# Performance work log

Measured on AMD Instinct MI355X. Metric: run time of the kernel, lower is better.

Reference implementation:

```python
import jax, jax.numpy as jnp
import numpy as np


def setup_inputs() -> dict:
    key = jax.random.key(0)
    k1, k2, k3 = jax.random.split(key, 3)
    B, C, Q, E = 32, 2048, 128, 200
    x_contexts = jax.random.normal(k1, (B, C, E), dtype=jnp.float32)
    x_questions = jax.random.normal(k2, (B, Q, E), dtype=jnp.float32)
    # weight of nn.Linear(3E, 1, bias=False), flattened to (3E,)
    w_sim = jax.random.normal(k3, (3 * E,), dtype=jnp.float32) * (1.0 / np.sqrt(3 * E))
    return {"x_contexts": x_contexts, "x_questions": x_questions, "w_sim": w_sim}


def reference(x_contexts, x_questions, w_sim):
    # x_contexts: [B,C,E], x_questions: [B,Q,E], w_sim: [3E]
    E = x_contexts.shape[-1]
    w1, w2, w3 = w_sim[:E], w_sim[E:2 * E], w_sim[2 * E:]
    # Trilinear similarity S[b,c,q] = w1.c + w2.q + w3.(c*q), decomposed so the
    # [B,C,Q,3E] tensor of the original expand+cat+linear is never materialized.
    s_c = jnp.einsum('bce,e->bc', x_contexts, w1)              # [B,C]
    s_q = jnp.einsum('bqe,e->bq', x_questions, w2)             # [B,Q]
    s_cq = jnp.einsum('bce,bqe->bcq', x_contexts * w3, x_questions)  # [B,C,Q]
    S = s_cq + s_c[:, :, None] + s_q[:, None, :]               # [B,C,Q]

    # Context-to-question: row softmax over Q, then attend over questions.
    c2q = jnp.einsum('bcq,bqe->bce', jax.nn.softmax(S, axis=-1), x_questions)

    # Question-to-context: max over Q, softmax over C, attend over contexts.
    q2c_w = jax.nn.softmax(jnp.max(S, axis=-1), axis=-1)       # [B,C]
    q2c = jnp.einsum('bc,bce->be', q2c_w, x_contexts)          # [B,E]
    q2c = q2c[:, None, :]                                      # broadcast to [B,C,E]

    return jnp.concatenate(
        [x_contexts, c2q, x_contexts * c2q, x_contexts * q2c], axis=-1)  # [B,C,4E]
```

## Files before the change

kernel.cpp:

```cpp
#include <hip/hip_runtime.h>

#define B_ 32
#define C_ 2048
#define Q_ 128
#define E_ 200
#define TB 32

typedef __attribute__((ext_vector_type(4))) float f32x4;

__global__ __launch_bounds__(256) void xqt_kernel(const float* __restrict__ xq,
                                                  float* __restrict__ xqT) {
    __shared__ float tl[32][33];
    const int blk = blockIdx.x;
    const int b  = blk / 28;
    const int r  = blk - b * 28;
    const int qt = r / 7, et = r - (r / 7) * 7;
    const int q0 = qt * 32, e0 = et * 32;
    const int tx = threadIdx.x & 31, ty = threadIdx.x >> 5;
    #pragma unroll
    for (int i = 0; i < 4; ++i) {
        const int q = q0 + ty + 8 * i, e = e0 + tx;
        if (e < E_) tl[ty + 8 * i][tx] = xq[((size_t)b * Q_ + q) * E_ + e];
    }
    __syncthreads();
    #pragma unroll
    for (int i = 0; i < 4; ++i) {
        const int e = e0 + ty + 8 * i, q = q0 + tx;
        if (e < E_) xqT[((size_t)b * E_ + e) * Q_ + q] = tl[tx][ty + 8 * i];
    }
}

__global__ __launch_bounds__(256) void sq_kernel(const float* __restrict__ xq,
                                                 const float* __restrict__ w,
                                                 float* __restrict__ sq) {
    const int wave = blockIdx.x * 4 + (threadIdx.x >> 6);
    const int lane = threadIdx.x & 63;
    const float* row = xq + (size_t)wave * E_;
    float a = 0.f;
    if (lane < 50) {
        const f32x4 v  = *(const f32x4*)&row[lane * 4];
        const f32x4 wv = *(const f32x4*)&w[E_ + lane * 4];
        a = (v.x * wv.x + v.y * wv.y) + (v.z * wv.z + v.w * wv.w);
    }
    #pragma unroll
    for (int off = 32; off; off >>= 1) a += __shfl_xor(a, off);
    if (lane == 0) sq[wave] = a;
}

__global__ __launch_bounds__(256) void row2_kernel(const float* __restrict__ xc_g,
                                                   const float* __restrict__ xq_g,
                                                   const float* __restrict__ xqT_g,
                                                   const float* __restrict__ w_g,
                                                   const float* __restrict__ sq_g,
                                                   float* __restrict__ m_g,
                                                   float* __restrict__ out) {
    __shared__ float scw3_l[TB][E_];
    __shared__ float P_l[TB][Q_];
    __shared__ float sc_l[TB];

    const int t    = threadIdx.x;
    const int b    = blockIdx.x >> 6;
    const int tile = blockIdx.x & 63;
    const int bc0  = b * C_ + tile * TB;

    {
        const int r  = t >> 3;
        const int k  = t & 7;
        const int e0 = k * 25;
        const float* xc_row = xc_g + (size_t)(bc0 + r) * E_;
        float p1 = 0.f;
        #pragma unroll
        for (int i = 0; i < 25; ++i) {
            const int e = e0 + i;
            const float v = xc_row[e];
            scw3_l[r][e] = v * w_g[2 * E_ + e];
            p1 = fmaf(v, w_g[e], p1);
        }
        p1 += __shfl_xor(p1, 1);
        p1 += __shfl_xor(p1, 2);
        p1 += __shfl_xor(p1, 4);
        if (k == 0) sc_l[r] = p1;
    }
    __syncthreads();

    const int qg = t & 31;
    const int cg = t >> 5;
    const int c4 = cg * 4;
    const int q4 = qg * 4;

    f32x4 acc[4] = {};
    const float* xqT_b = xqT_g + (size_t)b * E_ * Q_;
    for (int e = 0; e < E_; e += 4) {
        const f32x4 x0 = *(const f32x4*)&xqT_b[(e + 0) * Q_ + q4];
        const f32x4 x1 = *(const f32x4*)&xqT_b[(e + 1) * Q_ + q4];
        const f32x4 x2 = *(const f32x4*)&xqT_b[(e + 2) * Q_ + q4];
        const f32x4 x3 = *(const f32x4*)&xqT_b[(e + 3) * Q_ + q4];
        #pragma unroll
        for (int ci = 0; ci < 4; ++ci) {
            const f32x4 a = *(const f32x4*)&scw3_l[c4 + ci][e];
            acc[ci] += a.x * x0 + a.y * x1 + a.z * x2 + a.w * x3;
        }
    }

    const f32x4 sqv = *(const f32x4*)&sq_g[b * Q_ + q4];
    float mx[4], sm[4];
    #pragma unroll
    for (int ci = 0; ci < 4; ++ci) {
        acc[ci] += sc_l[c4 + ci] + sqv;
        mx[ci] = fmaxf(fmaxf(acc[ci].x, acc[ci].y), fmaxf(acc[ci].z, acc[ci].w));
    }
    #pragma unroll
    for (int off = 16; off; off >>= 1) {
        #pragma unroll
        for (int ci = 0; ci < 4; ++ci) mx[ci] = fmaxf(mx[ci], __shfl_xor(mx[ci], off));
    }
    if (qg == 0) {
        #pragma unroll
        for (int ci = 0; ci < 4; ++ci) m_g[bc0 + c4 + ci] = mx[ci];
    }
    #pragma unroll
    for (int ci = 0; ci < 4; ++ci) {
        f32x4 p;
        p.x = __expf(acc[ci].x - mx[ci]);
        p.y = __expf(acc[ci].y - mx[ci]);
        p.z = __expf(acc[ci].z - mx[ci]);
        p.w = __expf(acc[ci].w - mx[ci]);
        acc[ci] = p;
        sm[ci] = (p.x + p.y) + (p.z + p.w);
    }
    #pragma unroll
    for (int off = 16; off; off >>= 1) {
        #pragma unroll
        for (int ci = 0; ci < 4; ++ci) sm[ci] += __shfl_xor(sm[ci], off);
    }
    #pragma unroll
    for (int ci = 0; ci < 4; ++ci) {
        acc[ci] *= (1.f / sm[ci]);
        *(f32x4*)&P_l[c4 + ci][q4] = acc[ci];
    }
    __syncthreads();

    const float* xq_b = xq_g + (size_t)b * Q_ * E_;
    #pragma unroll
    for (int pass = 0; pass < 2; ++pass) {
        const int e4 = pass * 128 + q4;
        if (e4 < E_) {
            f32x4 o[4] = {};
            for (int q = 0; q < Q_; q += 4) {
                const f32x4 xv0 = *(const f32x4*)&xq_b[(q + 0) * E_ + e4];
                const f32x4 xv1 = *(const f32x4*)&xq_b[(q + 1) * E_ + e4];
                const f32x4 xv2 = *(const f32x4*)&xq_b[(q + 2) * E_ + e4];
                const f32x4 xv3 = *(const f32x4*)&xq_b[(q + 3) * E_ + e4];
                #pragma unroll
                for (int ci = 0; ci < 4; ++ci) {
                    const f32x4 p = *(const f32x4*)&P_l[c4 + ci][q];
                    o[ci] += p.x * xv0 + p.y * xv1 + p.z * xv2 + p.w * xv3;
                }
            }
            #pragma unroll
            for (int ci = 0; ci < 4; ++ci) {
                const size_t row = (size_t)(bc0 + c4 + ci);
                const f32x4 xcv = *(const f32x4*)&xc_g[row * E_ + e4];
                float* orow = out + row * (4 * E_);
                *(f32x4*)&orow[e4]          = xcv;
                *(f32x4*)&orow[E_ + e4]     = o[ci];
                *(f32x4*)&orow[2 * E_ + e4] = xcv * o[ci];
            }
        }
    }
}

__global__ __launch_bounds__(256) void q2c_partial(const float* __restrict__ xc_g,
                                                   const float* __restrict__ m_g,
                                                   float* __restrict__ part,
                                                   float* __restrict__ pmax,
                                                   float* __restrict__ psum) {
    __shared__ float wl[64];
    __shared__ float red;
    const int blk = blockIdx.x;
    const int b = blk >> 5, g = blk & 31;
    const int t = threadIdx.x;
    const int c0 = g * 64;

    const float v = (t < 64) ? m_g[b * C_ + c0 + t] : -3.4e38f;
    if (t < 64) {
        float mxl = v;
        #pragma unroll
        for (int off = 32; off; off >>= 1) mxl = fmaxf(mxl, __shfl_xor(mxl, off));
        const float e = __expf(v - mxl);
        wl[t] = e;
        float s = e;
        #pragma unroll
        for (int off = 32; off; off >>= 1) s += __shfl_xor(s, off);
        if (t == 0) { pmax[blk] = mxl; psum[blk] = s; red = mxl; }
    }
    __syncthreads();

    if (t < E_) {
        float acc = 0.f;
        const float* base = xc_g + ((size_t)(b * C_ + c0)) * E_ + t;
        #pragma unroll 8
        for (int c = 0; c < 64; ++c) acc = fmaf(wl[c], base[(size_t)c * E_], acc);
        part[(size_t)blk * E_ + t] = acc;
    }
}

__global__ __launch_bounds__(256) void q2c_reduce(const float* __restrict__ part,
                                                  const float* __restrict__ pmax,
                                                  const float* __restrict__ psum,
                                                  float* __restrict__ q2c) {
    __shared__ float sc[32];
    __shared__ float inv_total;
    const int b = blockIdx.x, t = threadIdx.x;
    if (t < 64) {
        const float pm = (t < 32) ? pmax[b * 32 + t] : -3.4e38f;
        float M = pm;
        #pragma unroll
        for (int off = 32; off; off >>= 1) M = fmaxf(M, __shfl_xor(M, off));
        const float s = (t < 32) ? __expf(pm - M) : 0.f;
        float tot = (t < 32) ? psum[b * 32 + t] * s : 0.f;
        #pragma unroll
        for (int off = 32; off; off >>= 1) tot += __shfl_xor(tot, off);
        if (t < 32) sc[t] = s;
        if (t == 0) inv_total = 1.f / tot;
    }
    __syncthreads();
    if (t < E_) {
        float a = 0.f;
        #pragma unroll
        for (int g = 0; g < 32; ++g)
            a = fmaf(part[(size_t)(b * 32 + g) * E_ + t], sc[g], a);
        q2c[b * E_ + t] = a * inv_total;
    }
}

__global__ __launch_bounds__(256) void out4_kernel(const float* __restrict__ xc_g,
                                                   const float* __restrict__ q2c,
                                                   float* __restrict__ out) {
    const unsigned int idx = blockIdx.x * 256u + threadIdx.x;
    const unsigned int n = idx * 4u;
    const unsigned int e = n % E_;
    const unsigned int row = n / E_;
    const unsigned int b = row / C_;
    const f32x4 xcv = *(const f32x4*)&xc_g[n];
    const f32x4 qv  = *(const f32x4*)&q2c[b * E_ + e];
    *(f32x4*)&out[(size_t)row * (4 * E_) + 3 * E_ + e] = xcv * qv;
}

extern "C" void kernel_launch(void* const* d_in, const int* in_sizes, int n_in,
                              void* d_out, int out_size, void* d_ws, size_t ws_size,
                              hipStream_t stream) {
    const float* xc = (const float*)d_in[0];
    const float* xq = (const float*)d_in[1];
    const float* w  = (const float*)d_in[2];
    for (int i = 0; i < n_in; ++i) {
        if      (in_sizes[i] == B_ * C_ * E_) xc = (const float*)d_in[i];
        else if (in_sizes[i] == B_ * Q_ * E_) xq = (const float*)d_in[i];
        else if (in_sizes[i] == 3 * E_)       w  = (const float*)d_in[i];
    }
    float* out = (float*)d_out;

    float* ws    = (float*)d_ws;
    float* sq    = ws;
    float* m     = sq + B_ * Q_;
    float* q2c   = m + B_ * C_;
    float* xqT   = q2c + B_ * E_;
    float* part  = xqT;
    float* pmax  = xqT + 262144;
    float* psum  = xqT + 262144 + 2048;

    xqt_kernel  <<<B_ * 28,            256, 0, stream>>>(xq, xqT);
    sq_kernel   <<<B_ * Q_ / 4,        256, 0, stream>>>(xq, w, sq);
    row2_kernel <<<B_ * (C_ / TB),     256, 0, stream>>>(xc, xq, xqT, w, sq, m, out);
    q2c_partial <<<B_ * 32,            256, 0, stream>>>(xc, m, part, pmax, psum);
    q2c_reduce  <<<B_,                 256, 0, stream>>>(part, pmax, psum, q2c);
    out4_kernel <<<(B_ * C_ * E_ / 4) / 256, 256, 0, stream>>>(xc, q2c, out);
}
```

Measured before the change: 407.6 us.

## Merge prep kernels, halve row tile, fold q2c reduce into output kernel

The transpose and s_q kernels become one launch, with the block index choosing the role. The main row kernel tile drops from 32 to 16 context rows per block, doubling the block count for occupancy at the cost of less reuse of xqT and xq per block. The q2c softmax now computes the global max inside each partial block, which removes the rescale pass, and the separate reduce kernel is folded into the final output kernel. This cuts launches and removes a tiny serial kernel, but each q2c_partial block now rereads all 2048 maxima for its batch and each out4 block rereads all 32 partials.

After: 515.6 us. 26.5% more time.

```diff
diff --git a/kernel.cpp b/kernel.cpp
--- a/kernel.cpp
+++ b/kernel.cpp
@@ -4,47 +4,47 @@
 #define C_ 2048
 #define Q_ 128
 #define E_ 200
-#define TB 32
+#define TB 16
 
 typedef __attribute__((ext_vector_type(4))) float f32x4;
 
-__global__ __launch_bounds__(256) void xqt_kernel(const float* __restrict__ xq,
-                                                  float* __restrict__ xqT) {
+__global__ __launch_bounds__(256) void prep_kernel(const float* __restrict__ xq,
+                                                   const float* __restrict__ w,
+                                                   float* __restrict__ xqT,
+                                                   float* __restrict__ sq) {
     __shared__ float tl[32][33];
-    const int blk = blockIdx.x;
-    const int b  = blk / 28;
-    const int r  = blk - b * 28;
-    const int qt = r / 7, et = r - (r / 7) * 7;
-    const int q0 = qt * 32, e0 = et * 32;
-    const int tx = threadIdx.x & 31, ty = threadIdx.x >> 5;
-    #pragma unroll
-    for (int i = 0; i < 4; ++i) {
-        const int q = q0 + ty + 8 * i, e = e0 + tx;
-        if (e < E_) tl[ty + 8 * i][tx] = xq[((size_t)b * Q_ + q) * E_ + e];
-    }
-    __syncthreads();
-    #pragma unroll
-    for (int i = 0; i < 4; ++i) {
-        const int e = e0 + ty + 8 * i, q = q0 + tx;
-        if (e < E_) xqT[((size_t)b * E_ + e) * Q_ + q] = tl[tx][ty + 8 * i];
-    }
-}
-
-__global__ __launch_bounds__(256) void sq_kernel(const float* __restrict__ xq,
-                                                 const float* __restrict__ w,
-                                                 float* __restrict__ sq) {
-    const int wave = blockIdx.x * 4 + (threadIdx.x >> 6);
-    const int lane = threadIdx.x & 63;
-    const float* row = xq + (size_t)wave * E_;
-    float a = 0.f;
-    if (lane < 50) {
-        const f32x4 v  = *(const f32x4*)&row[lane * 4];
-        const f32x4 wv = *(const f32x4*)&w[E_ + lane * 4];
-        a = (v.x * wv.x + v.y * wv.y) + (v.z * wv.z + v.w * wv.w);
-    }
-    #pragma unroll
-    for (int off = 32; off; off >>= 1) a += __shfl_xor(a, off);
-    if (lane == 0) sq[wave] = a;
+    if (blockIdx.x < 896) {
+        const int blk = blockIdx.x;
+        const int b  = blk / 28;
+        const int r  = blk - b * 28;
+        const int qt = r / 7, et = r - (r / 7) * 7;
+        const int q0 = qt * 32, e0 = et * 32;
+        const int tx = threadIdx.x & 31, ty = threadIdx.x >> 5;
+        #pragma unroll
+        for (int i = 0; i < 4; ++i) {
+            const int q = q0 + ty + 8 * i, e = e0 + tx;
+            if (e < E_) tl[ty + 8 * i][tx] = xq[((size_t)b * Q_ + q) * E_ + e];
+        }
+        __syncthreads();
+        #pragma unroll
+        for (int i = 0; i < 4; ++i) {
+            const int e = e0 + ty + 8 * i, q = q0 + tx;
+            if (e < E_) xqT[((size_t)b * E_ + e) * Q_ + q] = tl[tx][ty + 8 * i];
+        }
+    } else {
+        const int wave = (blockIdx.x - 896) * 4 + (threadIdx.x >> 6);
+        const int lane = threadIdx.x & 63;
+        const float* row = xq + (size_t)wave * E_;
+        float a = 0.f;
+        if (lane < 50) {
+            const f32x4 v  = *(const f32x4*)&row[lane * 4];
+            const f32x4 wv = *(const f32x4*)&w[E_ + lane * 4];
+            a = (v.x * wv.x + v.y * wv.y) + (v.z * wv.z + v.w * wv.w);
+        }
+        #pragma unroll
+        for (int off = 32; off; off >>= 1) a += __shfl_xor(a, off);
+        if (lane == 0) sq[wave] = a;
+    }
 }
 
 __global__ __launch_bounds__(256) void row2_kernel(const float* __restrict__ xc_g,
@@ -59,18 +59,18 @@
     __shared__ float sc_l[TB];
 
     const int t    = threadIdx.x;
-    const int b    = blockIdx.x >> 6;
-    const int tile = blockIdx.x & 63;
+    const int b    = blockIdx.x >> 7;
+    const int tile = blockIdx.x & 127;
     const int bc0  = b * C_ + tile * TB;
 
     {
-        const int r  = t >> 3;
-        const int k  = t & 7;
-        const int e0 = k * 25;
+        const int r   = t >> 4;
+        const int k   = t & 15;
+        const int e0  = (k < 8) ? k * 13 : 104 + (k - 8) * 12;
+        const int cnt = (k < 8) ? 13 : 12;
         const float* xc_row = xc_g + (size_t)(bc0 + r) * E_;
         float p1 = 0.f;
-        #pragma unroll
-        for (int i = 0; i < 25; ++i) {
+        for (int i = 0; i < cnt; ++i) {
             const int e = e0 + i;
             const float v = xc_row[e];
             scw3_l[r][e] = v * w_g[2 * E_ + e];
@@ -79,16 +79,17 @@
         p1 += __shfl_xor(p1, 1);
         p1 += __shfl_xor(p1, 2);
         p1 += __shfl_xor(p1, 4);
+        p1 += __shfl_xor(p1, 8);
         if (k == 0) sc_l[r] = p1;
     }
     __syncthreads();
 
     const int qg = t & 31;
     const int cg = t >> 5;
-    const int c4 = cg * 4;
+    const int c2 = cg * 2;
     const int q4 = qg * 4;
 
-    f32x4 acc[4] = {};
+    f32x4 acc[2] = {};
     const float* xqT_b = xqT_g + (size_t)b * E_ * Q_;
     for (int e = 0; e < E_; e += 4) {
         const f32x4 x0 = *(const f32x4*)&xqT_b[(e + 0) * Q_ + q4];
@@ -96,30 +97,30 @@
         const f32x4 x2 = *(const f32x4*)&xqT_b[(e + 2) * Q_ + q4];
         const f32x4 x3 = *(const f32x4*)&xqT_b[(e + 3) * Q_ + q4];
         #pragma unroll
-        for (int ci = 0; ci < 4; ++ci) {
-            const f32x4 a = *(const f32x4*)&scw3_l[c4 + ci][e];
+        for (int ci = 0; ci < 2; ++ci) {
+            const f32x4 a = *(const f32x4*)&scw3_l[c2 + ci][e];
             acc[ci] += a.x * x0 + a.y * x1 + a.z * x2 + a.w * x3;
         }
     }
 
     const f32x4 sqv = *(const f32x4*)&sq_g[b * Q_ + q4];
-    float mx[4], sm[4];
-    #pragma unroll
-    for (int ci = 0; ci < 4; ++ci) {
-        acc[ci] += sc_l[c4 + ci] + sqv;
+    float mx[2], sm[2];
+    #pragma unroll
+    for (int ci = 0; ci < 2; ++ci) {
+        acc[ci] += sc_l[c2 + ci] + sqv;
         mx[ci] = fmaxf(fmaxf(acc[ci].x, acc[ci].y), fmaxf(acc[ci].z, acc[ci].w));
     }
     #pragma unroll
     for (int off = 16; off; off >>= 1) {
         #pragma unroll
-        for (int ci = 0; ci < 4; ++ci) mx[ci] = fmaxf(mx[ci], __shfl_xor(mx[ci], off));
+        for (int ci = 0; ci < 2; ++ci) mx[ci] = fmaxf(mx[ci], __shfl_xor(mx[ci], off));
     }
     if (qg == 0) {
         #pragma unroll
-        for (int ci = 0; ci < 4; ++ci) m_g[bc0 + c4 + ci] = mx[ci];
-    }
-    #pragma unroll
-    for (int ci = 0; ci < 4; ++ci) {
+        for (int ci = 0; ci < 2; ++ci) m_g[bc0 + c2 + ci] = mx[ci];
+    }
+    #pragma unroll
+    for (int ci = 0; ci < 2; ++ci) {
         f32x4 p;
         p.x = __expf(acc[ci].x - mx[ci]);
         p.y = __expf(acc[ci].y - mx[ci]);
@@ -131,12 +132,12 @@
     #pragma unroll
     for (int off = 16; off; off >>= 1) {
         #pragma unroll
-        for (int ci = 0; ci < 4; ++ci) sm[ci] += __shfl_xor(sm[ci], off);
-    }
-    #pragma unroll
-    for (int ci = 0; ci < 4; ++ci) {
+        for (int ci = 0; ci < 2; ++ci) sm[ci] += __shfl_xor(sm[ci], off);
+    }
+    #pragma unroll
+    for (int ci = 0; ci < 2; ++ci) {
         acc[ci] *= (1.f / sm[ci]);
-        *(f32x4*)&P_l[c4 + ci][q4] = acc[ci];
+        *(f32x4*)&P_l[c2 + ci][q4] = acc[ci];
     }
     __syncthreads();
 
@@ -145,21 +146,21 @@
     for (int pass = 0; pass < 2; ++pass) {
         const int e4 = pass * 128 + q4;
         if (e4 < E_) {
-            f32x4 o[4] = {};
+            f32x4 o[2] = {};
             for (int q = 0; q < Q_; q += 4) {
                 const f32x4 xv0 = *(const f32x4*)&xq_b[(q + 0) * E_ + e4];
                 const f32x4 xv1 = *(const f32x4*)&xq_b[(q + 1) * E_ + e4];
                 const f32x4 xv2 = *(const f32x4*)&xq_b[(q + 2) * E_ + e4];
                 const f32x4 xv3 = *(const f32x4*)&xq_b[(q + 3) * E_ + e4];
                 #pragma unroll
-                for (int ci = 0; ci < 4; ++ci) {
-                    const f32x4 p = *(const f32x4*)&P_l[c4 + ci][q];
+                for (int ci = 0; ci < 2; ++ci) {
+                    const f32x4 p = *(const f32x4*)&P_l[c2 + ci][q];
                     o[ci] += p.x * xv0 + p.y * xv1 + p.z * xv2 + p.w * xv3;
                 }
             }
             #pragma unroll
-            for (int ci = 0; ci < 4; ++ci) {
-                const size_t row = (size_t)(bc0 + c4 + ci);
+            for (int ci = 0; ci < 2; ++ci) {
+                const size_t row = (size_t)(bc0 + c2 + ci);
                 const f32x4 xcv = *(const f32x4*)&xc_g[row * E_ + e4];
                 float* orow = out + row * (4 * E_);
                 *(f32x4*)&orow[e4]          = xcv;
@@ -173,26 +174,30 @@
 __global__ __launch_bounds__(256) void q2c_partial(const float* __restrict__ xc_g,
                                                    const float* __restrict__ m_g,
                                                    float* __restrict__ part,
-                                                   float* __restrict__ pmax,
-                                                   float* __restrict__ psum) {
+                                                   float* __restrict__ den) {
+    __shared__ float redl[4];
     __shared__ float wl[64];
-    __shared__ float red;
     const int blk = blockIdx.x;
     const int b = blk >> 5, g = blk & 31;
     const int t = threadIdx.x;
     const int c0 = g * 64;
 
-    const float v = (t < 64) ? m_g[b * C_ + c0 + t] : -3.4e38f;
+    float mx = -3.4e38f;
+    #pragma unroll
+    for (int j = 0; j < 8; ++j) mx = fmaxf(mx, m_g[b * C_ + t + j * 256]);
+    #pragma unroll
+    for (int off = 32; off; off >>= 1) mx = fmaxf(mx, __shfl_xor(mx, off));
+    if ((t & 63) == 0) redl[t >> 6] = mx;
+    __syncthreads();
+    const float M = fmaxf(fmaxf(redl[0], redl[1]), fmaxf(redl[2], redl[3]));
+
     if (t < 64) {
-        float mxl = v;
-        #pragma unroll
-        for (int off = 32; off; off >>= 1) mxl = fmaxf(mxl, __shfl_xor(mxl, off));
-        const float e = __expf(v - mxl);
+        const float e = __expf(m_g[b * C_ + c0 + t] - M);
         wl[t] = e;
         float s = e;
         #pragma unroll
         for (int off = 32; off; off >>= 1) s += __shfl_xor(s, off);
-        if (t == 0) { pmax[blk] = mxl; psum[blk] = s; red = mxl; }
+        if (t == 0) den[blk] = s;
     }
     __syncthreads();
 
@@ -205,46 +210,43 @@
     }
 }
 
-__global__ __launch_bounds__(256) void q2c_reduce(const float* __restrict__ part,
-                                                  const float* __restrict__ pmax,
-                                                  const float* __restrict__ psum,
-                                                  float* __restrict__ q2c) {
-    __shared__ float sc[32];
-    __shared__ float inv_total;
-    const int b = blockIdx.x, t = threadIdx.x;
-    if (t < 64) {
-        const float pm = (t < 32) ? pmax[b * 32 + t] : -3.4e38f;
-        float M = pm;
-        #pragma unroll
-        for (int off = 32; off; off >>= 1) M = fmaxf(M, __shfl_xor(M, off));
-        const float s = (t < 32) ? __expf(pm - M) : 0.f;
-        float tot = (t < 32) ? psum[b * 32 + t] * s : 0.f;
-        #pragma unroll
-        for (int off = 32; off; off >>= 1) tot += __shfl_xor(tot, off);
-        if (t < 32) sc[t] = s;
-        if (t == 0) inv_total = 1.f / tot;
-    }
-    __syncthreads();
+__global__ __launch_bounds__(256) void out4_kernel(const float* __restrict__ xc_g,
+                                                   const float* __restrict__ part,
+                                                   const float* __restrict__ den,
+                                                   float* __restrict__ out) {
+    __shared__ float q2c_l[E_];
+    __shared__ float invt;
+    const int blk = blockIdx.x;
+    const int b = blk >> 5, g = blk & 31;
+    const int c0 = g * 64;
+    const int t = threadIdx.x;
+
     if (t < E_) {
         float a = 0.f;
         #pragma unroll
-        for (int g = 0; g < 32; ++g)
-            a = fmaf(part[(size_t)(b * 32 + g) * E_ + t], sc[g], a);
-        q2c[b * E_ + t] = a * inv_total;
-    }
-}
-
-__global__ __launch_bounds__(256) void out4_kernel(const float* __restrict__ xc_g,
-                                                   const float* __restrict__ q2c,
-                                                   float* __restrict__ out) {
-    const unsigned int idx = blockIdx.x * 256u + threadIdx.x;
-    const unsigned int n = idx * 4u;
-    const unsigned int e = n % E_;
-    const unsigned int row = n / E_;
-    const unsigned int b = row / C_;
-    const f32x4 xcv = *(const f32x4*)&xc_g[n];
-    const f32x4 qv  = *(const f32x4*)&q2c[b * E_ + e];
-    *(f32x4*)&out[(size_t)row * (4 * E_) + 3 * E_ + e] = xcv * qv;
+        for (int gg = 0; gg < 32; ++gg) a += part[(size_t)(b * 32 + gg) * E_ + t];
+        q2c_l[t] = a;
+    }
+    if (t >= 224) {
+        float s = den[b * 32 + (t - 224)];
+        #pragma unroll
+        for (int off = 16; off; off >>= 1) s += __shfl_xor(s, off);
+        if (t == 224) invt = 1.f / s;
+    }
+    __syncthreads();
+
+    const float iv = invt;
+    const int e4 = (t % 50) * 4;
+    const int r0 = t / 50;
+    if (t < 200) {
+        #pragma unroll
+        for (int kk = 0; kk < 16; ++kk) {
+            const size_t row = (size_t)(b * C_ + c0 + kk * 4 + r0);
+            const f32x4 xcv = *(const f32x4*)&xc_g[row * E_ + e4];
+            const f32x4 qv  = *(const f32x4*)&q2c_l[e4];
+            *(f32x4*)&out[row * (4 * E_) + 3 * E_ + e4] = xcv * (qv * iv);
+        }
+    }
 }
 
 extern "C" void kernel_launch(void* const* d_in, const int* in_sizes, int n_in,
@@ -263,16 +265,12 @@
     float* ws    = (float*)d_ws;
     float* sq    = ws;
     float* m     = sq + B_ * Q_;
-    float* q2c   = m + B_ * C_;
-    float* xqT   = q2c + B_ * E_;
+    float* xqT   = m + B_ * C_;
     float* part  = xqT;
-    float* pmax  = xqT + 262144;
-    float* psum  = xqT + 262144 + 2048;
-
-    xqt_kernel  <<<B_ * 28,            256, 0, stream>>>(xq, xqT);
-    sq_kernel   <<<B_ * Q_ / 4,        256, 0, stream>>>(xq, w, sq);
+    float* den   = xqT + 1024 * E_;
+
+    prep_kernel <<<1920,               256, 0, stream>>>(xq, w, xqT, sq);
     row2_kernel <<<B_ * (C_ / TB),     256, 0, stream>>>(xc, xq, xqT, w, sq, m, out);
-    q2c_partial <<<B_ * 32,            256, 0, stream>>>(xc, m, part, pmax, psum);
-    q2c_reduce  <<<B_,                 256, 0, stream>>>(part, pmax, psum, q2c);
-    out4_kernel <<<(B_ * C_ * E_ / 4) / 256, 256, 0, stream>>>(xc, q2c, out);
-}
+    q2c_partial <<<B_ * 32,            256, 0, stream>>>(xc, m, part, den);
+    out4_kernel <<<B_ * 32,            256, 0, stream>>>(xc, part, den, out);
+}
```
